# Optimization experiments

Measured on AMD Instinct MI355X. Metric: run time of the kernel, lower is better.

Reference implementation:

```python
import jax, jax.numpy as jnp
import numpy as np

DIM = 1024
EXPAND = 1.5
D_INNER = int(EXPAND * DIM)  # 1536
B, L = 4, 4096


def setup_inputs() -> dict:
    key = jax.random.key(0)
    ks = jax.random.split(key, 9)
    x = jax.random.normal(ks[0], (B, L, DIM), dtype=jnp.float32)
    # Linear weights stored torch-style: (out_features, in_features)
    W_in = jax.random.normal(ks[1], (D_INNER * 2, DIM), dtype=jnp.float32) / np.sqrt(DIM)
    W_out = jax.random.normal(ks[2], (DIM, D_INNER), dtype=jnp.float32) / np.sqrt(D_INNER)
    conv_w = jax.random.normal(ks[3], (D_INNER, 1, 3), dtype=jnp.float32) / np.sqrt(3.0)
    conv_b = jax.random.normal(ks[4], (D_INNER,), dtype=jnp.float32) * 0.01
    dt_w = jax.random.normal(ks[5], (D_INNER, D_INNER), dtype=jnp.float32) / np.sqrt(D_INNER)
    dt_b = jnp.zeros((D_INNER,), dtype=jnp.float32)
    # A initialized as -rand*0.1 (strictly negative, matches torch init)
    A = -jax.random.uniform(ks[6], (D_INNER,), dtype=jnp.float32) * 0.1
    Dp = jnp.ones((D_INNER,), dtype=jnp.float32)
    return {"x": x, "W_in": W_in, "W_out": W_out, "conv_w": conv_w,
            "conv_b": conv_b, "dt_w": dt_w, "dt_b": dt_b, "A": A, "Dp": Dp}


def _forward(x, W_in, W_out, conv_w, conv_b, dt_w, dt_b, A, Dp):
    # in_proj: (B,L,D) @ (D, 2*d_inner)
    xz = jnp.einsum('bld,ed->ble', x, W_in)
    x_inner, z = jnp.split(xz, 2, axis=-1)
    # depthwise conv1d, kernel=3, padding=1
    xc = jnp.transpose(x_inner, (0, 2, 1))  # (B, C, L)
    xc = jax.lax.conv_general_dilated(
        xc, conv_w, window_strides=(1,), padding=[(1, 1)],
        dimension_numbers=('NCH', 'OIH', 'NCH'),
        feature_group_count=D_INNER)
    xc = xc + conv_b[None, :, None]
    x_conv = jax.nn.silu(jnp.transpose(xc, (0, 2, 1)))  # (B, L, C)
    dt = jax.nn.softplus(jnp.einsum('blc,ec->ble', x_conv, dt_w) + dt_b)
    A_exp = jnp.exp(A[None, None, :] * dt)
    x_weighted = x_conv * dt
    y = jnp.cumsum(x_weighted * A_exp, axis=1) * A_exp
    y = y + x_conv * Dp[None, None, :]
    y = y * jax.nn.silu(z)
    return jnp.einsum('blc,dc->bld', y, W_out)


def reference(x, W_in, W_out, conv_w, conv_b, dt_w, dt_b, A, Dp):
    return _forward(x, W_in, W_out, conv_w, conv_b, dt_w, dt_b, A, Dp)
```

## Files before the change

kernel.cpp:

```cpp
#include <hip/hip_runtime.h>
#include <cstdint>
#include <cstddef>

#define L_SEQ   4096
#define DIM_IN  1024
#define DI      1536
#define BATCH   4

typedef unsigned short u16;
typedef __attribute__((ext_vector_type(8))) short  short8;
typedef __attribute__((ext_vector_type(4))) float  f32x4;

struct __align__(8) u16x4 { u16 x, y, z, w; };

__device__ __forceinline__ float bf2f(u16 u) {
  union { unsigned int i; float f; } v; v.i = ((unsigned int)u) << 16; return v.f;
}
__device__ __forceinline__ u16 f2bf(float f) {
  union { float f; unsigned int i; } v; v.f = f;
  unsigned int x = v.i;
  return (u16)((x + 0x7fffu + ((x >> 16) & 1u)) >> 16);
}
__device__ __forceinline__ float siluf_(float v) {
  return v / (1.0f + __expf(-v));
}
__device__ __forceinline__ float softplusf_(float v) {
  return fmaxf(v, 0.0f) + log1pf(__expf(-fabsf(v)));
}
__device__ __forceinline__ void gload16(const void* g, void* l) {
  __builtin_amdgcn_global_load_lds((const __attribute__((address_space(1))) void*)g,
                                   (__attribute__((address_space(3))) void*)l,
                                   16, 0, 0);
}

__global__ void to_bf16(const float* __restrict__ in, u16* __restrict__ out, int n4) {
  int i = blockIdx.x * blockDim.x + threadIdx.x;
  if (i >= n4) return;
  float4 v = ((const float4*)in)[i];
  u16x4 o;
  o.x = f2bf(v.x); o.y = f2bf(v.y); o.z = f2bf(v.z); o.w = f2bf(v.w);
  ((u16x4*)out)[i] = o;
}

template <int EPI>
__launch_bounds__(256, 3)
__global__ void gemm_bt(const u16* __restrict__ A, const u16* __restrict__ Bt,
                        float* __restrict__ c_out,
                        int N, int K,
                        u16* __restrict__ e_bf_a,
                        u16* __restrict__ e_bf1,
                        const u16* __restrict__ e_bf2,
                        const float* __restrict__ e_v1,
                        const float* __restrict__ e_v2) {
  __shared__ u16 Alds[128 * 64];
  __shared__ u16 Blds[128 * 64];

  const int tid  = threadIdx.x;
  const int wave = tid >> 6;
  const int lane = tid & 63;
  const int quad = lane >> 4;
  const int l16  = lane & 15;

  const int nwg  = (int)(gridDim.x * gridDim.y);
  const int orig = (int)(blockIdx.y * gridDim.x + blockIdx.x);
  const int swz  = (orig & 7) * (nwg >> 3) + (orig >> 3);
  const int bx   = swz % (int)gridDim.x;
  const int by   = swz / (int)gridDim.x;
  const int m0 = by * 128;
  const int n0 = bx * 128;

  const int waveM = wave & 1;
  const int waveN = wave >> 1;

  const int srow = tid >> 3;
  const int scol = ((tid & 7) ^ (srow & 7)) * 8;
  const u16* Ap = A  + (size_t)(m0 + srow) * K + scol;
  const u16* Bp = Bt + (size_t)(n0 + srow) * K + scol;
  u16* adst = &Alds[tid * 8];
  u16* bdst = &Blds[tid * 8];

  const unsigned xorc = (unsigned)(l16 & 7) << 3;

  f32x4 acc[4][4] = {};

  for (int k0 = 0; k0 < K; k0 += 64) {
#pragma unroll
    for (int r = 0; r < 4; ++r) {
      gload16(Ap + (size_t)(r * 32) * K + k0, adst + r * 2048);
      gload16(Bp + (size_t)(r * 32) * K + k0, bdst + r * 2048);
    }
    __syncthreads();

#pragma unroll
    for (int kb = 0; kb < 2; ++kb) {
      short8 af[4], bf[4];
      const unsigned ck = (unsigned)(kb * 32 + quad * 8) ^ xorc;
#pragma unroll
      for (int i = 0; i < 4; i++) {
        af[i] = *(const short8*)&Alds[(unsigned)(waveM * 64 + i * 16 + l16) * 64 + ck];
        bf[i] = *(const short8*)&Blds[(unsigned)(waveN * 64 + i * 16 + l16) * 64 + ck];
      }
#pragma unroll
      for (int mi = 0; mi < 4; mi++)
#pragma unroll
        for (int ni = 0; ni < 4; ni++)
          acc[mi][ni] = __builtin_amdgcn_mfma_f32_16x16x32_bf16(af[mi], bf[ni],
                                                                acc[mi][ni], 0, 0, 0);
    }
    __syncthreads();
  }

#pragma unroll
  for (int mi = 0; mi < 4; mi++) {
    const int rowBase = m0 + waveM * 64 + mi * 16 + quad * 4;
#pragma unroll
    for (int ni = 0; ni < 4; ni++) {
      const int gcol = n0 + waveN * 64 + ni * 16 + l16;
#pragma unroll
      for (int r = 0; r < 4; r++) {
        const float v = acc[mi][ni][r];
        const size_t row = (size_t)(rowBase + r);
        if constexpr (EPI == 0) {
          c_out[row * (size_t)N + gcol] = v;
        } else if constexpr (EPI == 1) {
          if (gcol < DI) {
            e_bf_a[row * DI + gcol] = f2bf(v);
          } else {
            e_bf1[row * DI + (gcol - DI)] = f2bf(siluf_(v));
          }
        } else {
          const float dt = softplusf_(v + e_v2[gcol]);
          const float a  = __expf(e_v1[gcol] * dt);
          const float xc = bf2f(e_bf2[row * DI + gcol]);
          e_bf_a[row * DI + gcol] = f2bf(xc * dt * a);
          e_bf1[row * DI + gcol] = f2bf(a);
        }
      }
    }
  }
}

__global__ void conv_silu(const u16* __restrict__ xin, const float* __restrict__ cw,
                          const float* __restrict__ cb, u16* __restrict__ xconv_bf) {
  const int idx = blockIdx.x * blockDim.x + threadIdx.x;
  const int c4  = (idx % (DI / 4)) * 4;
  const int row = idx / (DI / 4);
  const int l   = row & (L_SEQ - 1);

  const size_t base = (size_t)row * DI + c4;
  u16x4 z4 = {0, 0, 0, 0};
  u16x4 x1 = *(const u16x4*)(xin + base);
  u16x4 x0 = (l > 0)         ? *(const u16x4*)(xin + base - DI) : z4;
  u16x4 x2 = (l < L_SEQ - 1) ? *(const u16x4*)(xin + base + DI) : z4;

  const u16* p0 = (const u16*)&x0;
  const u16* p1 = (const u16*)&x1;
  const u16* p2 = (const u16*)&x2;
  u16x4 o;
  u16* po = (u16*)&o;
#pragma unroll
  for (int j = 0; j < 4; j++) {
    const int c = c4 + j;
    float v = fmaf(cw[c * 3 + 0], bf2f(p0[j]),
              fmaf(cw[c * 3 + 1], bf2f(p1[j]),
                   cw[c * 3 + 2] * bf2f(p2[j]))) + cb[c];
    po[j] = f2bf(siluf_(v));
  }
  *(u16x4*)&xconv_bf[base] = o;
}

#define CHUNK 128
#define NCHUNK (L_SEQ / CHUNK)

__global__ void scan_partial(const u16* __restrict__ w, float* __restrict__ partial) {
  const int c  = blockIdx.x * 256 + threadIdx.x;
  const int ch = blockIdx.y;
  const int b  = blockIdx.z;
  size_t base = ((size_t)b * L_SEQ + (size_t)ch * CHUNK) * DI + c;
  float s = 0.0f;
#pragma unroll 4
  for (int i = 0; i < CHUNK; i++) s += bf2f(w[base + (size_t)i * DI]);
  partial[((size_t)b * NCHUNK + ch) * DI + c] = s;
}

__global__ void scan_offsets(float* __restrict__ partial) {
  const int c = blockIdx.x * 256 + threadIdx.x;
  const int b = blockIdx.z;
  float run = 0.0f;
  for (int ch = 0; ch < NCHUNK; ch++) {
    size_t p = ((size_t)b * NCHUNK + ch) * DI + c;
    float v = partial[p];
    partial[p] = run;
    run += v;
  }
}

__global__ void scan_apply(const u16* __restrict__ w, const float* __restrict__ partial,
                           const u16* aexp, const u16* __restrict__ xconv,
                           const u16* __restrict__ sz, const float* __restrict__ Dp,
                           u16* ybf) {
  const int c  = blockIdx.x * 256 + threadIdx.x;
  const int ch = blockIdx.y;
  const int b  = blockIdx.z;
  float run = partial[((size_t)b * NCHUNK + ch) * DI + c];
  const float dp = Dp[c];
  size_t base = ((size_t)b * L_SEQ + (size_t)ch * CHUNK) * DI + c;
  for (int i = 0; i < CHUNK; i++) {
    size_t p = base + (size_t)i * DI;
    float ae = bf2f(aexp[p]);
    run += bf2f(w[p]);
    float y = run * ae + bf2f(xconv[p]) * dp;
    y *= bf2f(sz[p]);
    ybf[p] = f2bf(y);
  }
}

extern "C" void kernel_launch(void* const* d_in, const int* in_sizes, int n_in,
                              void* d_out, int out_size, void* d_ws, size_t ws_size,
                              hipStream_t stream) {
  const float* x      = (const float*)d_in[0];
  const float* W_in   = (const float*)d_in[1];
  const float* W_out  = (const float*)d_in[2];
  const float* conv_w = (const float*)d_in[3];
  const float* conv_b = (const float*)d_in[4];
  const float* dt_w   = (const float*)d_in[5];
  const float* dt_b   = (const float*)d_in[6];
  const float* Avec   = (const float*)d_in[7];
  const float* Dp     = (const float*)d_in[8];
  float* out = (float*)d_out;
  char* ws = (char*)d_ws;

  u16* Win_bf  = (u16*)(ws + 0);
  u16* dtw_bf  = (u16*)(ws + 6291456);
  u16* Wout_bf = (u16*)(ws + 11010048);
  to_bf16<<<3072, 256, 0, stream>>>(W_in,  Win_bf,  786432);
  to_bf16<<<2304, 256, 0, stream>>>(dt_w,  dtw_bf,  589824);
  to_bf16<<<1536, 256, 0, stream>>>(W_out, Wout_bf, 393216);

  const size_t FULL_NEED = 249823232;
  if (ws_size >= FULL_NEED) {
    u16*   x_bf     = (u16*)  (ws + 14155776);
    u16*   xin_bf   = (u16*)  (ws + 47710208);
    u16*   sz_bf    = (u16*)  (ws + 98041856);
    u16*   xconv_bf = (u16*)  (ws + 148373504);
    u16*   aexp_bf  = (u16*)  (ws + 198705152);
    float* part     = (float*)(ws + 249036800);
    u16*   w_bf     = xin_bf;
    u16*   y_bf     = aexp_bf;

    to_bf16<<<16384, 256, 0, stream>>>(x, x_bf, 4194304);

    gemm_bt<1><<<dim3(24, 128), 256, 0, stream>>>(x_bf, Win_bf, nullptr,
                                                  2 * DI, DIM_IN,
                                                  xin_bf, sz_bf, nullptr, nullptr, nullptr);
    conv_silu<<<24576, 256, 0, stream>>>(xin_bf, conv_w, conv_b, xconv_bf);

    gemm_bt<2><<<dim3(12, 128), 256, 0, stream>>>(xconv_bf, dtw_bf, nullptr,
                                                  DI, DI,
                                                  w_bf, aexp_bf, xconv_bf, Avec, dt_b);

    scan_partial<<<dim3(6, NCHUNK, BATCH), 256, 0, stream>>>(w_bf, part);
    scan_offsets<<<dim3(6, 1, BATCH), 256, 0, stream>>>(part);
    scan_apply<<<dim3(6, NCHUNK, BATCH), 256, 0, stream>>>(w_bf, part, aexp_bf,
                                                           xconv_bf, sz_bf, Dp, y_bf);

    gemm_bt<0><<<dim3(8, 128), 256, 0, stream>>>(y_bf, Wout_bf, out,
                                                 DIM_IN, DI,
                                                 nullptr, nullptr, nullptr, nullptr, nullptr);
    return;
  }

  const size_t WS_NEED = 73072640;
  if (ws_size < WS_NEED) return;

  u16*   x_bf     = (u16*)  (ws + 14155776);
  u16*   xin_bf   = (u16*)  (ws + 22544384);
  u16*   sz_bf    = (u16*)  (ws + 35127296);
  u16*   xconv_bf = (u16*)  (ws + 47710208);
  u16*   aexp_bf  = (u16*)  (ws + 60293120);
  float* part     = (float*)(ws + 72876032);
  u16*   w_bf     = xin_bf;
  u16*   y_bf     = aexp_bf;

  for (int b = 0; b < BATCH; b++) {
    const float* xb   = x   + (size_t)b * L_SEQ * DIM_IN;
    float*       outb = out + (size_t)b * L_SEQ * DIM_IN;

    to_bf16<<<4096, 256, 0, stream>>>(xb, x_bf, 1048576);
    gemm_bt<1><<<dim3(24, 32), 256, 0, stream>>>(x_bf, Win_bf, nullptr,
                                                 2 * DI, DIM_IN,
                                                 xin_bf, sz_bf, nullptr, nullptr, nullptr);
    conv_silu<<<6144, 256, 0, stream>>>(xin_bf, conv_w, conv_b, xconv_bf);
    gemm_bt<2><<<dim3(12, 32), 256, 0, stream>>>(xconv_bf, dtw_bf, nullptr,
                                                 DI, DI,
                                                 w_bf, aexp_bf, xconv_bf, Avec, dt_b);
    scan_partial<<<dim3(6, NCHUNK, 1), 256, 0, stream>>>(w_bf, part);
    scan_offsets<<<dim3(6, 1, 1), 256, 0, stream>>>(part);
    scan_apply<<<dim3(6, NCHUNK, 1), 256, 0, stream>>>(w_bf, part, aexp_bf,
                                                       xconv_bf, sz_bf, Dp, y_bf);
    gemm_bt<0><<<dim3(8, 32), 256, 0, stream>>>(y_bf, Wout_bf, outb,
                                                DIM_IN, DI,
                                                nullptr, nullptr, nullptr, nullptr, nullptr);
  }
}
```

Baseline: 567.0 us.

## Add 256x256 pipelined MFMA GEMM for in_proj and fold scan offsets into apply

Adds a new 512-thread GEMM kernel with 256x256 tiles, double-buffered LDS staged by global_load_lds, XOR-swizzled ds_read_b128, interleaved MFMA phases with setprio, and a workgroup swizzle for L2 locality. It replaces the 128-tile in_proj GEMM on the full-workspace path to raise data reuse and overlap loads with compute. It also removes the serial scan_offsets launch, so each scan_apply block sums the preceding chunk partials itself. This saves one launch at the cost of redundant partial reads. The new GEMM relies on hand-written waitcnt and barrier ordering, which is fragile.

Result: slower. 596.1 us (+5.1%).

```diff
diff --git a/kernel.cpp b/kernel.cpp
--- a/kernel.cpp
+++ b/kernel.cpp
@@ -32,6 +32,15 @@
                                    (__attribute__((address_space(3))) void*)l,
                                    16, 0, 0);
 }
+__device__ __forceinline__ unsigned lds_off(const void* p) {
+  return (unsigned)(uintptr_t)(const __attribute__((address_space(3))) void*)p;
+}
+__device__ __forceinline__ short8 dsread128(unsigned off) {
+  short8 r;
+  asm volatile("ds_read_b128 %0, %1" : "=v"(r) : "v"(off));
+  return r;
+}
+#define RAW_BARRIER() asm volatile("s_barrier" ::: "memory")
 
 __global__ void to_bf16(const float* __restrict__ in, u16* __restrict__ out, int n4) {
   int i = blockIdx.x * blockDim.x + threadIdx.x;
@@ -40,6 +49,150 @@
   u16x4 o;
   o.x = f2bf(v.x); o.y = f2bf(v.y); o.z = f2bf(v.z); o.w = f2bf(v.w);
   ((u16x4*)out)[i] = o;
+}
+
+__device__ __forceinline__ void mma_ph8(f32x4 (&acc)[4][8], const short8 (&a)[4][2],
+                                        const short8 (&b)[2][2], int p) {
+#pragma unroll
+  for (int kb = 0; kb < 2; ++kb)
+#pragma unroll
+    for (int i = 0; i < 4; ++i)
+#pragma unroll
+      for (int n = 0; n < 2; ++n)
+        acc[i][p * 2 + n] = __builtin_amdgcn_mfma_f32_16x16x32_bf16(a[i][kb], b[n][kb],
+                                                                    acc[i][p * 2 + n], 0, 0, 0);
+}
+
+__launch_bounds__(512, 2)
+__global__ void gemm256(const u16* __restrict__ A, const u16* __restrict__ Bt,
+                        int N, int K,
+                        u16* __restrict__ e_bf_a,
+                        u16* __restrict__ e_bf1) {
+  __shared__ u16 smem[2][2][256 * 64];
+
+  const int tid  = threadIdx.x;
+  const int wave = tid >> 6;
+  const int lane = tid & 63;
+  const int quad = lane >> 4;
+  const int l16  = lane & 15;
+  const int waveM = wave & 3;
+  const int waveN = wave >> 2;
+  const int xorc  = (l16 & 7) << 3;
+
+  const int nwg  = (int)(gridDim.x * gridDim.y);
+  const int orig = (int)(blockIdx.y * gridDim.x + blockIdx.x);
+  const int swz  = (orig & 7) * (nwg >> 3) + (orig >> 3);
+  const int bx   = swz % (int)gridDim.x;
+  const int by   = swz / (int)gridDim.x;
+  const int m0 = by * 256;
+  const int n0 = bx * 256;
+  const int NT = K >> 6;
+
+  const int srow = tid >> 3;
+  const int scol = ((tid & 7) ^ (srow & 7)) * 8;
+  const u16* gA = A  + (size_t)(m0 + srow) * K + scol;
+  const u16* gB = Bt + (size_t)(n0 + srow) * K + scol;
+
+#define STAGE2(gptr, mat, kk, r0, r1) do {                                      \
+    const u16* _s0 = gptr + (size_t)(r0) * K + (size_t)(kk) * 64;               \
+    const u16* _s1 = gptr + (size_t)(r1) * K + (size_t)(kk) * 64;               \
+    gload16(_s0, &smem[(kk) & 1][mat][((r0) + wave * 8) * 64]);                 \
+    gload16(_s1, &smem[(kk) & 1][mat][((r1) + wave * 8) * 64]);                 \
+  } while (0)
+#define STAGE_A(kk, h) STAGE2(gA, 0, kk, (h) * 128, (h) * 128 + 64)
+#define STAGE_B(kk, h) STAGE2(gB, 1, kk, (h) * 64, (h) * 64 + 128)
+
+  STAGE_A(0, 0); STAGE_A(0, 1); STAGE_B(0, 0); STAGE_B(0, 1);
+  if (NT > 1) { STAGE_A(1, 0); STAGE_A(1, 1); STAGE_B(1, 0); }
+  if (NT > 1) asm volatile("s_waitcnt vmcnt(6)" ::: "memory");
+  else        asm volatile("s_waitcnt vmcnt(0)" ::: "memory");
+  RAW_BARRIER();
+
+  f32x4 acc[4][8] = {};
+  short8 a[4][2], b[2][2];
+
+  const unsigned ldsBase = lds_off(&smem[0][0][0]);
+  const unsigned rowA = (unsigned)(waveM * 64 + l16) * 128u;
+  const unsigned rowB = (unsigned)(waveN * 128 + l16) * 128u;
+  const unsigned ck0  = (unsigned)(((0 * 32 + quad * 8) ^ xorc) * 2);
+  const unsigned ck1  = (unsigned)(((1 * 32 + quad * 8) ^ xorc) * 2);
+
+#define LDB8(Bc, p) do {                                                        \
+    const unsigned _rb = (Bc) + rowB + (unsigned)(p) * 4096u;                   \
+    b[0][0] = dsread128(_rb + ck0);                                             \
+    b[0][1] = dsread128(_rb + ck1);                                             \
+    b[1][0] = dsread128(_rb + 2048u + ck0);                                     \
+    b[1][1] = dsread128(_rb + 2048u + ck1);                                     \
+  } while (0)
+#define WAIT_LGKM() do {                                                        \
+    asm volatile("s_waitcnt lgkmcnt(0)" ::: "memory");                          \
+    __builtin_amdgcn_sched_barrier(0);                                          \
+  } while (0)
+#define PH_TAIL(p) do {                                                         \
+    RAW_BARRIER();                                                              \
+    WAIT_LGKM();                                                                \
+    __builtin_amdgcn_s_setprio(1);                                              \
+    mma_ph8(acc, a, b, p);                                                      \
+    __builtin_amdgcn_s_setprio(0);                                              \
+    RAW_BARRIER();                                                              \
+  } while (0)
+
+  for (int t = 0; t < NT; ++t) {
+    const int cur = t & 1;
+    const bool s1 = (t + 1 < NT);
+    const bool s2 = (t + 2 < NT);
+    const unsigned Ac = ldsBase + (unsigned)cur * 65536u;
+    const unsigned Bc = Ac + 32768u;
+
+#pragma unroll
+    for (int i = 0; i < 4; ++i) {
+      const unsigned ra = Ac + rowA + (unsigned)i * 2048u;
+      a[i][0] = dsread128(ra + ck0);
+      a[i][1] = dsread128(ra + ck1);
+    }
+    LDB8(Bc, 0);
+    if (s1) STAGE_B(t + 1, 1);
+    PH_TAIL(0);
+
+    LDB8(Bc, 1);
+    if (s2) STAGE_A(t + 2, 0);
+    PH_TAIL(1);
+
+    LDB8(Bc, 2);
+    if (s2) STAGE_A(t + 2, 1);
+    PH_TAIL(2);
+
+    LDB8(Bc, 3);
+    if (s2) {
+      STAGE_B(t + 2, 0);
+      asm volatile("s_waitcnt vmcnt(6)" ::: "memory");
+    } else {
+      asm volatile("s_waitcnt vmcnt(0)" ::: "memory");
+    }
+    PH_TAIL(3);
+  }
+#undef STAGE_A
+#undef STAGE_B
+#undef STAGE2
+#undef LDB8
+#undef WAIT_LGKM
+#undef PH_TAIL
+
+#pragma unroll
+  for (int mi = 0; mi < 4; ++mi) {
+    const int rowBase = m0 + waveM * 64 + mi * 16 + quad * 4;
+#pragma unroll
+    for (int ni = 0; ni < 8; ++ni) {
+      const int gcol = n0 + waveN * 128 + ni * 16 + l16;
+#pragma unroll
+      for (int r = 0; r < 4; ++r) {
+        const float v = acc[mi][ni][r];
+        const size_t row = (size_t)(rowBase + r);
+        if (gcol < DI) e_bf_a[row * DI + gcol] = f2bf(v);
+        else           e_bf1[row * DI + (gcol - DI)] = f2bf(siluf_(v));
+      }
+    }
+  }
 }
 
 template <int EPI>
@@ -183,18 +336,6 @@
   partial[((size_t)b * NCHUNK + ch) * DI + c] = s;
 }
 
-__global__ void scan_offsets(float* __restrict__ partial) {
-  const int c = blockIdx.x * 256 + threadIdx.x;
-  const int b = blockIdx.z;
-  float run = 0.0f;
-  for (int ch = 0; ch < NCHUNK; ch++) {
-    size_t p = ((size_t)b * NCHUNK + ch) * DI + c;
-    float v = partial[p];
-    partial[p] = run;
-    run += v;
-  }
-}
-
 __global__ void scan_apply(const u16* __restrict__ w, const float* __restrict__ partial,
                            const u16* aexp, const u16* __restrict__ xconv,
                            const u16* __restrict__ sz, const float* __restrict__ Dp,
@@ -202,7 +343,9 @@
   const int c  = blockIdx.x * 256 + threadIdx.x;
   const int ch = blockIdx.y;
   const int b  = blockIdx.z;
-  float run = partial[((size_t)b * NCHUNK + ch) * DI + c];
+  float run = 0.0f;
+  for (int j = 0; j < ch; ++j)
+    run += partial[((size_t)b * NCHUNK + j) * DI + c];
   const float dp = Dp[c];
   size_t base = ((size_t)b * L_SEQ + (size_t)ch * CHUNK) * DI + c;
   for (int i = 0; i < CHUNK; i++) {
@@ -250,9 +393,9 @@
 
     to_bf16<<<16384, 256, 0, stream>>>(x, x_bf, 4194304);
 
-    gemm_bt<1><<<dim3(24, 128), 256, 0, stream>>>(x_bf, Win_bf, nullptr,
-                                                  2 * DI, DIM_IN,
-                                                  xin_bf, sz_bf, nullptr, nullptr, nullptr);
+    gemm256<<<dim3(12, 64), 512, 0, stream>>>(x_bf, Win_bf,
+                                              2 * DI, DIM_IN,
+                                              xin_bf, sz_bf);
     conv_silu<<<24576, 256, 0, stream>>>(xin_bf, conv_w, conv_b, xconv_bf);
 
     gemm_bt<2><<<dim3(12, 128), 256, 0, stream>>>(xconv_bf, dtw_bf, nullptr,
@@ -260,7 +403,6 @@
                                                   w_bf, aexp_bf, xconv_bf, Avec, dt_b);
 
     scan_partial<<<dim3(6, NCHUNK, BATCH), 256, 0, stream>>>(w_bf, part);
-    scan_offsets<<<dim3(6, 1, BATCH), 256, 0, stream>>>(part);
     scan_apply<<<dim3(6, NCHUNK, BATCH), 256, 0, stream>>>(w_bf, part, aexp_bf,
                                                            xconv_bf, sz_bf, Dp, y_bf);
 
@@ -295,7 +437,6 @@
                                                  DI, DI,
                                                  w_bf, aexp_bf, xconv_bf, Avec, dt_b);
     scan_partial<<<dim3(6, NCHUNK, 1), 256, 0, stream>>>(w_bf, part);
-    scan_offsets<<<dim3(6, 1, 1), 256, 0, stream>>>(part);
     scan_apply<<<dim3(6, NCHUNK, 1), 256, 0, stream>>>(w_bf, part, aexp_bf,
                                                        xconv_bf, sz_bf, Dp, y_bf);
     gemm_bt<0><<<dim3(8, 32), 256, 0, stream>>>(y_bf, Wout_bf, outb,
```

## Fuse scan chunk partial sums into dt GEMM epilogue, drop scan kernels

Applied to the files above, without the earlier changes.

The dt GEMM epilogue now sums its weighted values per column over each 128-row tile, using shuffles plus a small LDS reduction, and writes per-chunk partial sums. This removes the separate scan_partial and scan_offsets kernels, so the weighted tensor is not read back a second time. scan_apply now computes its prefix offset by looping over the earlier chunk partials itself. The partials are summed in fp32 before bf16 rounding, which changes numerics slightly, and the offset loop adds up to 31 extra loads per thread.

Result: slower. 588.0 us (+3.7%).

```diff
diff --git a/kernel.cpp b/kernel.cpp
--- a/kernel.cpp
+++ b/kernel.cpp
@@ -51,7 +51,8 @@
                         u16* __restrict__ e_bf1,
                         const u16* __restrict__ e_bf2,
                         const float* __restrict__ e_v1,
-                        const float* __restrict__ e_v2) {
+                        const float* __restrict__ e_v2,
+                        float* __restrict__ e_part) {
   __shared__ u16 Alds[128 * 64];
   __shared__ u16 Blds[128 * 64];
 
@@ -110,6 +111,7 @@
     __syncthreads();
   }
 
+  float colsum[4] = {0.0f, 0.0f, 0.0f, 0.0f};
 #pragma unroll
   for (int mi = 0; mi < 4; mi++) {
     const int rowBase = m0 + waveM * 64 + mi * 16 + quad * 4;
@@ -132,9 +134,34 @@
           const float dt = softplusf_(v + e_v2[gcol]);
           const float a  = __expf(e_v1[gcol] * dt);
           const float xc = bf2f(e_bf2[row * DI + gcol]);
-          e_bf_a[row * DI + gcol] = f2bf(xc * dt * a);
+          const float w  = xc * dt * a;
+          e_bf_a[row * DI + gcol] = f2bf(w);
           e_bf1[row * DI + gcol] = f2bf(a);
+          colsum[ni] += w;
         }
+      }
+    }
+  }
+
+  if constexpr (EPI == 2) {
+#pragma unroll
+    for (int ni = 0; ni < 4; ++ni) {
+      colsum[ni] += __shfl_xor(colsum[ni], 16);
+      colsum[ni] += __shfl_xor(colsum[ni], 32);
+    }
+    float* red = (float*)&Alds[0];
+    if (waveM == 0 && quad == 0) {
+#pragma unroll
+      for (int ni = 0; ni < 4; ++ni)
+        red[(waveN * 4 + ni) * 16 + l16] = colsum[ni];
+    }
+    __syncthreads();
+    if (waveM == 1 && quad == 0) {
+      const int chunk = m0 >> 7;
+#pragma unroll
+      for (int ni = 0; ni < 4; ++ni) {
+        const int c = n0 + waveN * 64 + ni * 16 + l16;
+        e_part[(size_t)chunk * DI + c] = colsum[ni] + red[(waveN * 4 + ni) * 16 + l16];
       }
     }
   }
@@ -171,29 +198,6 @@
 
 #define CHUNK 128
 #define NCHUNK (L_SEQ / CHUNK)
-
-__global__ void scan_partial(const u16* __restrict__ w, float* __restrict__ partial) {
-  const int c  = blockIdx.x * 256 + threadIdx.x;
-  const int ch = blockIdx.y;
-  const int b  = blockIdx.z;
-  size_t base = ((size_t)b * L_SEQ + (size_t)ch * CHUNK) * DI + c;
-  float s = 0.0f;
-#pragma unroll 4
-  for (int i = 0; i < CHUNK; i++) s += bf2f(w[base + (size_t)i * DI]);
-  partial[((size_t)b * NCHUNK + ch) * DI + c] = s;
-}
-
-__global__ void scan_offsets(float* __restrict__ partial) {
-  const int c = blockIdx.x * 256 + threadIdx.x;
-  const int b = blockIdx.z;
-  float run = 0.0f;
-  for (int ch = 0; ch < NCHUNK; ch++) {
-    size_t p = ((size_t)b * NCHUNK + ch) * DI + c;
-    float v = partial[p];
-    partial[p] = run;
-    run += v;
-  }
-}
 
 __global__ void scan_apply(const u16* __restrict__ w, const float* __restrict__ partial,
                            const u16* aexp, const u16* __restrict__ xconv,
@@ -202,7 +206,9 @@
   const int c  = blockIdx.x * 256 + threadIdx.x;
   const int ch = blockIdx.y;
   const int b  = blockIdx.z;
-  float run = partial[((size_t)b * NCHUNK + ch) * DI + c];
+  float run = 0.0f;
+  for (int j = 0; j < ch; ++j)
+    run += partial[((size_t)b * NCHUNK + j) * DI + c];
   const float dp = Dp[c];
   size_t base = ((size_t)b * L_SEQ + (size_t)ch * CHUNK) * DI + c;
   for (int i = 0; i < CHUNK; i++) {
@@ -252,21 +258,22 @@
 
     gemm_bt<1><<<dim3(24, 128), 256, 0, stream>>>(x_bf, Win_bf, nullptr,
                                                   2 * DI, DIM_IN,
-                                                  xin_bf, sz_bf, nullptr, nullptr, nullptr);
+                                                  xin_bf, sz_bf, nullptr, nullptr, nullptr,
+                                                  nullptr);
     conv_silu<<<24576, 256, 0, stream>>>(xin_bf, conv_w, conv_b, xconv_bf);
 
     gemm_bt<2><<<dim3(12, 128), 256, 0, stream>>>(xconv_bf, dtw_bf, nullptr,
                                                   DI, DI,
-                                                  w_bf, aexp_bf, xconv_bf, Avec, dt_b);
-
-    scan_partial<<<dim3(6, NCHUNK, BATCH), 256, 0, stream>>>(w_bf, part);
-    scan_offsets<<<dim3(6, 1, BATCH), 256, 0, stream>>>(part);
+                                                  w_bf, aexp_bf, xconv_bf, Avec, dt_b,
+                                                  part);
+
     scan_apply<<<dim3(6, NCHUNK, BATCH), 256, 0, stream>>>(w_bf, part, aexp_bf,
                                                            xconv_bf, sz_bf, Dp, y_bf);
 
     gemm_bt<0><<<dim3(8, 128), 256, 0, stream>>>(y_bf, Wout_bf, out,
                                                  DIM_IN, DI,
-                                                 nullptr, nullptr, nullptr, nullptr, nullptr);
+                                                 nullptr, nullptr, nullptr, nullptr, nullptr,
+                                                 nullptr);
     return;
   }
 
@@ -289,17 +296,18 @@
     to_bf16<<<4096, 256, 0, stream>>>(xb, x_bf, 1048576);
     gemm_bt<1><<<dim3(24, 32), 256, 0, stream>>>(x_bf, Win_bf, nullptr,
                                                  2 * DI, DIM_IN,
-                                                 xin_bf, sz_bf, nullptr, nullptr, nullptr);
+                                                 xin_bf, sz_bf, nullptr, nullptr, nullptr,
+                                                 nullptr);
     conv_silu<<<6144, 256, 0, stream>>>(xin_bf, conv_w, conv_b, xconv_bf);
     gemm_bt<2><<<dim3(12, 32), 256, 0, stream>>>(xconv_bf, dtw_bf, nullptr,
                                                  DI, DI,
-                                                 w_bf, aexp_bf, xconv_bf, Avec, dt_b);
-    scan_partial<<<dim3(6, NCHUNK, 1), 256, 0, stream>>>(w_bf, part);
-    scan_offsets<<<dim3(6, 1, 1), 256, 0, stream>>>(part);
+                                                 w_bf, aexp_bf, xconv_bf, Avec, dt_b,
+                                                 part);
     scan_apply<<<dim3(6, NCHUNK, 1), 256, 0, stream>>>(w_bf, part, aexp_bf,
                                                        xconv_bf, sz_bf, Dp, y_bf);
     gemm_bt<0><<<dim3(8, 32), 256, 0, stream>>>(y_bf, Wout_bf, outb,
                                                 DIM_IN, DI,
-                                                nullptr, nullptr, nullptr, nullptr, nullptr);
-  }
-}
+                                                nullptr, nullptr, nullptr, nullptr, nullptr,
+                                                nullptr);
+  }
+}
```
